# Kernel optimization log

Measured on AMD Instinct MI355X. Metric: run time of the kernel, lower is better.

Reference implementation:

```python
import jax, jax.numpy as jnp
import numpy as np

NM, C_IN, T, V = 256, 64, 128, 21
C_OUT = 64
N_CONVS = 3  # forward only uses convs[0..2]
EPS_BN = 1e-5


def _build_edges(nm, t):
    # replicates get_hi(): 6x6 incidence (transposed), tiled over NM*T graphs
    inc = np.array([[1, 0, 0, 0, 1, 0],
                    [1, 1, 0, 0, 0, 1],
                    [1, 0, 1, 0, 0, 1],
                    [1, 0, 0, 1, 0, 0],
                    [1, 0, 0, 0, 1, 0],
                    [0, 1, 1, 0, 0, 1]], dtype=np.int64).T
    r_idx, c_idx = np.nonzero(inc)  # row-major order, matches torch nonzero
    g = nm * t                      # num_graphs
    nnz = len(r_idx)                # 14
    row = np.tile(r_idx, g) + np.repeat(np.arange(g), nnz) * 6   # targets (edge-node ids)
    col = np.tile(c_idx, g) + np.repeat(np.arange(g), nnz) * 21  # sources (vertex ids)
    return jnp.asarray(col, jnp.int32), jnp.asarray(row, jnp.int32)


def setup_inputs() -> dict:
    key = jax.random.key(0)
    ks = jax.random.split(key, 8)
    x = jax.random.normal(ks[0], (NM, C_IN, T, V), dtype=jnp.float32)
    src, dst = _build_edges(NM, T)
    s_in = 1.0 / np.sqrt(C_IN)
    s_att = 1.0 / np.sqrt(C_OUT)
    Wl = jax.random.normal(ks[1], (N_CONVS, C_OUT, C_IN), jnp.float32) * s_in
    bl = jnp.zeros((N_CONVS, C_OUT), jnp.float32)
    Wr = jax.random.normal(ks[2], (N_CONVS, C_OUT, C_IN), jnp.float32) * s_in
    br = jnp.zeros((N_CONVS, C_OUT), jnp.float32)
    att = jax.random.normal(ks[3], (N_CONVS, C_OUT), jnp.float32) * s_att
    bias = jnp.zeros((N_CONVS, C_OUT), jnp.float32)
    gamma = jnp.full((C_OUT,), 1e-6, jnp.float32)  # bn_init(self.bn, 1e-6)
    beta = jnp.zeros((C_OUT,), jnp.float32)
    return {"x": x, "src": src, "dst": dst, "Wl": Wl, "bl": bl, "Wr": Wr,
            "br": br, "att": att, "bias": bias, "gamma": gamma, "beta": beta}


def _gatv2(feat, src_all, dst_all, valid, Wl, bl, Wr, br, att, bias, n):
    # GATv2Conv, heads=1: e_ij = att . LeakyReLU(Wl x_j + Wr x_i); softmax over dst
    xl = feat @ Wl.T + bl           # [N, Cout]
    xr = feat @ Wr.T + br           # [N, Cout]
    msg = xl[src_all]               # [E, Cout]
    e = jax.nn.leaky_relu(msg + xr[dst_all], 0.2) @ att  # [E]
    e = jnp.where(valid, e, -1e9)   # removed self-loops excluded
    m = jax.ops.segment_max(e, dst_all, num_segments=n)
    a = jnp.exp(e - m[dst_all]) * valid
    denom = jax.ops.segment_sum(a, dst_all, num_segments=n)
    a = a / denom[dst_all]
    return jax.ops.segment_sum(a[:, None] * msg, dst_all, num_segments=n) + bias


def reference(x, src, dst, Wl, bl, Wr, br, att, bias, gamma, beta):
    nm, c, t, v = x.shape
    n = nm * t * v
    feat = jnp.transpose(x, (0, 2, 3, 1)).reshape(n, c)  # '(nm t v) c'
    # PyG GATv2: remove existing self-loops, then add self-loops for all N nodes
    loop = jnp.arange(n, dtype=src.dtype)
    src_all = jnp.concatenate([src, loop])
    dst_all = jnp.concatenate([dst, loop])
    valid = jnp.concatenate([src != dst, jnp.ones((n,), bool)])
    y = None
    for i in range(N_CONVS):
        z = _gatv2(feat, src_all, dst_all, valid,
                   Wl[i], bl[i], Wr[i], br[i], att[i], bias[i], n)
        y = z if y is None else y + z
    y = y.reshape(nm, C_OUT, t, v)  # matches torch .view on node-major buffer
    # BatchNorm2d (eval, running mean 0 / var 1), gamma initialized to 1e-6
    y = y / jnp.sqrt(1.0 + EPS_BN) * gamma[None, :, None, None] + beta[None, :, None, None]
    return jax.nn.relu(y + x)  # residual identity (in_channels == out_channels)
```

## Files before the change

### kernel.cpp

```cpp
#include <hip/hip_runtime.h>
#include <hip/hip_bf16.h>

#define NMSLICE 2688
#define NMELEMS 172032
#define NNODE   688128
#define NDST    196608
#define BNRS    0.9999950000374996f

typedef __attribute__((ext_vector_type(8))) _Float16 half8;
typedef __attribute__((ext_vector_type(2))) _Float16 half2v;
typedef __attribute__((ext_vector_type(4))) unsigned uintx4;
typedef __attribute__((ext_vector_type(4))) float  floatx4;

__device__ __forceinline__ short h2s(float f) {
    union { _Float16 h; short s; } c;
    c.h = (_Float16)f;
    return c.s;
}

__device__ __forceinline__ void loadrow_h(const short* buf, int row, int cb, half2v* o) {
    #pragma unroll
    for (int h = 0; h < 2; ++h) {
        const int k8 = cb * 2 + h;
        uintx4 v = *reinterpret_cast<const uintx4*>(&buf[row * 64 + ((k8 ^ (row & 7)) << 3)]);
        #pragma unroll
        for (int j = 0; j < 4; ++j) o[h * 4 + j] = __builtin_bit_cast(half2v, v[j]);
    }
}

__device__ __forceinline__ float edot2(const half2v* a, const half2v* xr, const half2v* m) {
    half2v s = { (_Float16)0, (_Float16)0 };
    const half2v c02 = { (_Float16)0.2f, (_Float16)0.2f };
    #pragma unroll
    for (int j = 0; j < 8; ++j) {
        half2v z = m[j] + xr[j];
        z = __builtin_elementwise_max(z, c02 * z);
        s += a[j] * z;
    }
    float e = (float)s[0] + (float)s[1];
    e += __shfl_xor(e, 1);
    e += __shfl_xor(e, 2);
    return e;
}

__global__ void __launch_bounds__(256) prep_weights(
    const float* __restrict__ Wl, const float* __restrict__ Wr,
    const float* __restrict__ bl, const float* __restrict__ bias,
    const float* __restrict__ att,
    short* __restrict__ wfrag, float* __restrict__ csum, float* __restrict__ bsum,
    short* __restrict__ att_h)
{
    const int task = blockIdx.x * 256 + threadIdx.x;
    const int lane = task & 63;
    const int ks   = (task >> 6) & 1;
    const int nt   = (task >> 7) & 3;
    const int m    = task >> 9;
    const int co = nt * 16 + (lane & 15);
    const int k0 = ks * 32 + (lane >> 4) * 8;
    short v[8];
    if (m < 6) {
        const int cv = m >> 1;
        const float* W = (m & 1) ? (Wr + cv * 4096) : (Wl + cv * 4096);
        #pragma unroll
        for (int j = 0; j < 8; ++j) v[j] = h2s(W[co * 64 + k0 + j]);
    } else {
        #pragma unroll
        for (int j = 0; j < 8; ++j)
            v[j] = h2s(Wl[co*64 + k0 + j] + Wl[4096 + co*64 + k0 + j] + Wl[8192 + co*64 + k0 + j]);
    }
    #pragma unroll
    for (int j = 0; j < 8; ++j) wfrag[task * 8 + j] = v[j];
    if (blockIdx.x == 0 && threadIdx.x < 192) {
        const int t = threadIdx.x;
        att_h[t] = h2s(att[t]);
        if (t < 64) {
            csum[t] = bl[t] + bl[64+t] + bl[128+t] + bias[t] + bias[64+t] + bias[128+t];
            bsum[t] = bias[t] + bias[64+t] + bias[128+t];
        }
    }
}

__global__ void __launch_bounds__(256) gat_heavy(
    const float* __restrict__ x,
    const short* __restrict__ wfrag,
    const float* __restrict__ bl, const float* __restrict__ br,
    const short* __restrict__ att_h, const float* __restrict__ bsum,
    const float* __restrict__ gamma, const float* __restrict__ beta,
    float* __restrict__ out)
{
    __shared__ short XL[4 * 48 * 64];
    __shared__ short XR[4 * 24 * 64];

    const int lane = threadIdx.x & 63;
    const int wave = threadIdx.x >> 6;
    const int sbid = ((blockIdx.x & 7) << 8) + (blockIdx.x >> 3);
    const int W  = sbid * 4 + wave;
    const int n0 = W * 24;
    const int s0 = W * 84;

    short* XLw = XL + wave * (48 * 64);
    short* XRw = XR + wave * (24 * 64);

    const int nmD = n0 / NMSLICE, rmD = n0 - nmD * NMSLICE;
    const int nmS = s0 / NMSLICE, rmS = s0 - nmS * NMSLICE;

    #pragma unroll
    for (int i = 0; i < 6; ++i) {
        const int task = i * 64 + lane;
        const int r  = task % 48;
        const int k8 = task / 48;
        const float* bp;
        if (r < 24) {
            bp = x + (size_t)nmD * NMELEMS + rmD + r;
        } else {
            const int s = r - 24, gl = s / 6;
            bp = x + (size_t)nmS * NMELEMS + rmS + gl * 21 + (s - gl * 6);
        }
        short v[8];
        #pragma unroll
        for (int j = 0; j < 8; ++j) v[j] = h2s(bp[(size_t)(k8 * 8 + j) * NMSLICE]);
        *reinterpret_cast<half8*>(&XLw[r * 64 + ((k8 ^ (r & 7)) << 3)]) =
            *reinterpret_cast<half8*>(v);
    }

    const int l15 = lane & 15, l4 = lane >> 4;

    half8 aA[3][2];
    #pragma unroll
    for (int t = 0; t < 3; ++t) {
        const int arow = t * 16 + l15;
        #pragma unroll
        for (int ks = 0; ks < 2; ++ks)
            aA[t][ks] = *reinterpret_cast<const half8*>(
                &XLw[arow * 64 + (((ks * 4 + l4) ^ (arow & 7)) << 3)]);
    }

    const int ndA = lane >> 2, cbA = lane & 3;
    const int ndB = 16 + (lane >> 2), cbB = lane & 3;
    const unsigned long long TBL =
        31ull | (34ull << 8) | (36ull << 16) | (8ull << 24) | (17ull << 32) | (38ull << 40);
    const int glA = ndA / 6, rrA = ndA - glA * 6, srowA = 24 + glA * 6;
    const int glB = ndB / 6, rrB = ndB - glB * 6, srowB = 24 + glB * 6;
    unsigned maskA = (unsigned)((TBL >> (rrA * 8)) & 63u);
    unsigned maskB = (unsigned)((TBL >> (rrB * 8)) & 63u);
    if (W == 0 && glA == 0) maskA &= ~(1u << rrA);

    half2v yA2[8], yB2[8];
    #pragma unroll
    for (int j = 0; j < 8; ++j) {
        yA2[j] = half2v{ (_Float16)0, (_Float16)0 };
        yB2[j] = half2v{ (_Float16)0, (_Float16)0 };
    }

    for (int cv = 0; cv < 3; ++cv) {
        #pragma unroll
        for (int nt = 0; nt < 4; ++nt) {
            const int co = nt * 16 + l15;
            const short* wbL = wfrag + (size_t)(((cv * 2    ) * 4 + nt) * 2) * 512;
            const short* wbR = wfrag + (size_t)(((cv * 2 + 1) * 4 + nt) * 2) * 512;
            half8 wl0 = *reinterpret_cast<const half8*>(wbL + lane * 8);
            half8 wl1 = *reinterpret_cast<const half8*>(wbL + 512 + lane * 8);
            half8 wr0 = *reinterpret_cast<const half8*>(wbR + lane * 8);
            half8 wr1 = *reinterpret_cast<const half8*>(wbR + 512 + lane * 8);
            const float biL = bl[cv * 64 + co];
            const float biR = br[cv * 64 + co];
            #pragma unroll
            for (int u = 0; u < 3; ++u) {
                floatx4 acc = { biL, biL, biL, biL };
                acc = __builtin_amdgcn_mfma_f32_16x16x32_f16(aA[u][0], wl0, acc, 0, 0, 0);
                acc = __builtin_amdgcn_mfma_f32_16x16x32_f16(aA[u][1], wl1, acc, 0, 0, 0);
                #pragma unroll
                for (int qq = 0; qq < 4; ++qq) {
                    const int row = u * 16 + l4 * 4 + qq;
                    XLw[row * 64 + (((co >> 3) ^ (row & 7)) << 3) + (co & 7)] = h2s(acc[qq]);
                }
            }
            #pragma unroll
            for (int mtx = 0; mtx < 2; ++mtx) {
                floatx4 acc = { biR, biR, biR, biR };
                acc = __builtin_amdgcn_mfma_f32_16x16x32_f16(aA[mtx][0], wr0, acc, 0, 0, 0);
                acc = __builtin_amdgcn_mfma_f32_16x16x32_f16(aA[mtx][1], wr1, acc, 0, 0, 0);
                #pragma unroll
                for (int qq = 0; qq < 4; ++qq) {
                    const int row = mtx * 16 + l4 * 4 + qq;
                    if (row < 24)
                        XRw[row * 64 + (((co >> 3) ^ (row & 7)) << 3) + (co & 7)] = h2s(acc[qq]);
                }
            }
        }

        {
            half2v a2[8], xr2[8], m2[8], o2[8];
            {
                const uintx4* ap = reinterpret_cast<const uintx4*>(att_h + cv * 64 + cbA * 16);
                uintx4 v0 = ap[0], v1 = ap[1];
                #pragma unroll
                for (int j = 0; j < 4; ++j) {
                    a2[j]     = __builtin_bit_cast(half2v, v0[j]);
                    a2[4 + j] = __builtin_bit_cast(half2v, v1[j]);
                }
            }
            loadrow_h(XRw, ndA, cbA, xr2);
            loadrow_h(XLw, ndA, cbA, m2);
            float e = edot2(a2, xr2, m2);
            float w = __expf(e);
            float denom = w;
            half2v w2 = { (_Float16)w, (_Float16)w };
            #pragma unroll
            for (int j = 0; j < 8; ++j) o2[j] = w2 * m2[j];
            #pragma unroll
            for (int c = 0; c < 6; ++c) {
                loadrow_h(XLw, srowA + c, cbA, m2);
                e = edot2(a2, xr2, m2);
                w = (maskA & (1u << c)) ? __expf(e) : 0.f;
                denom += w;
                w2[0] = (_Float16)w; w2[1] = (_Float16)w;
                #pragma unroll
                for (int j = 0; j < 8; ++j) o2[j] += w2 * m2[j];
            }
            const _Float16 invh = (_Float16)(1.0f / denom);
            const half2v inv2 = { invh, invh };
            #pragma unroll
            for (int j = 0; j < 8; ++j) yA2[j] += inv2 * o2[j];
        }
        if (lane < 32) {
            half2v a2[8], xr2[8], m2[8], o2[8];
            {
                const uintx4* ap = reinterpret_cast<const uintx4*>(att_h + cv * 64 + cbB * 16);
                uintx4 v0 = ap[0], v1 = ap[1];
                #pragma unroll
                for (int j = 0; j < 4; ++j) {
                    a2[j]     = __builtin_bit_cast(half2v, v0[j]);
                    a2[4 + j] = __builtin_bit_cast(half2v, v1[j]);
                }
            }
            loadrow_h(XRw, ndB, cbB, xr2);
            loadrow_h(XLw, ndB, cbB, m2);
            float e = edot2(a2, xr2, m2);
            float w = __expf(e);
            float denom = w;
            half2v w2 = { (_Float16)w, (_Float16)w };
            #pragma unroll
            for (int j = 0; j < 8; ++j) o2[j] = w2 * m2[j];
            #pragma unroll
            for (int c = 0; c < 6; ++c) {
                loadrow_h(XLw, srowB + c, cbB, m2);
                e = edot2(a2, xr2, m2);
                w = (maskB & (1u << c)) ? __expf(e) : 0.f;
                denom += w;
                w2[0] = (_Float16)w; w2[1] = (_Float16)w;
                #pragma unroll
                for (int j = 0; j < 8; ++j) o2[j] += w2 * m2[j];
            }
            const _Float16 invh = (_Float16)(1.0f / denom);
            const half2v inv2 = { invh, invh };
            #pragma unroll
            for (int j = 0; j < 8; ++j) yB2[j] += inv2 * o2[j];
        }
    }

    {
        const size_t i0 = (size_t)(n0 + ndA) * 64 + cbA * 16;
        const int cobn = ((rmD + ndA) * 64 + cbA * 16) / NMSLICE;
        const float sc = gamma[cobn] * BNRS;
        const float bt = beta[cobn];
        #pragma unroll
        for (int j4 = 0; j4 < 4; ++j4) {
            floatx4 xv = *reinterpret_cast<const floatx4*>(x + i0 + j4 * 4);
            floatx4 ov;
            #pragma unroll
            for (int j = 0; j < 4; ++j) {
                const int jj = j4 * 4 + j;
                const float yv = (float)yA2[jj >> 1][jj & 1];
                float val = fmaf(yv + bsum[cbA * 16 + jj], sc, bt) + xv[j];
                ov[j] = fmaxf(val, 0.f);
            }
            *reinterpret_cast<floatx4*>(out + i0 + j4 * 4) = ov;
        }
    }
    if (lane < 32) {
        const size_t i0 = (size_t)(n0 + ndB) * 64 + cbB * 16;
        const int cobn = ((rmD + ndB) * 64 + cbB * 16) / NMSLICE;
        const float sc = gamma[cobn] * BNRS;
        const float bt = beta[cobn];
        #pragma unroll
        for (int j4 = 0; j4 < 4; ++j4) {
            floatx4 xv = *reinterpret_cast<const floatx4*>(x + i0 + j4 * 4);
            floatx4 ov;
            #pragma unroll
            for (int j = 0; j < 4; ++j) {
                const int jj = j4 * 4 + j;
                const float yv = (float)yB2[jj >> 1][jj & 1];
                float val = fmaf(yv + bsum[cbB * 16 + jj], sc, bt) + xv[j];
                ov[j] = fmaxf(val, 0.f);
            }
            *reinterpret_cast<floatx4*>(out + i0 + j4 * 4) = ov;
        }
    }
}

__global__ void __launch_bounds__(256) gat_light(
    const float* __restrict__ x,
    const short* __restrict__ wfrag,
    const float* __restrict__ csum,
    const float* __restrict__ gamma, const float* __restrict__ beta,
    float* __restrict__ out)
{
    __shared__ short F[256 * 64];

    const int t  = threadIdx.x;
    const int n0 = NDST + blockIdx.x * 256;

    {
        const int node = n0 + t;
        const int nm = node / NMSLICE;
        const int rm = node - nm * NMSLICE;
        const float* bp = x + (size_t)nm * NMELEMS + rm;
        #pragma unroll
        for (int k8 = 0; k8 < 8; ++k8) {
            short v[8];
            #pragma unroll
            for (int j = 0; j < 8; ++j) v[j] = h2s(bp[(size_t)(k8 * 8 + j) * NMSLICE]);
            *reinterpret_cast<half8*>(&F[t * 64 + ((k8 ^ (t & 7)) << 3)]) =
                *reinterpret_cast<half8*>(v);
        }
    }
    __syncthreads();

    const int wave = t >> 6, lane = t & 63;
    const int l15 = lane & 15, l4 = lane >> 4;
    const int rm0 = n0 % NMSLICE;
    #pragma unroll
    for (int ti = 0; ti < 16; ++ti) {
        const int tile = wave * 16 + ti;
        const int mt = tile >> 2, nt = tile & 3;
        const int co = nt * 16 + l15;
        const float bi = csum[co];
        floatx4 acc = { bi, bi, bi, bi };
        const short* wbase = wfrag + (size_t)((6 * 4 + nt) * 2) * 512;
        const int arow = mt * 16 + l15;
        #pragma unroll
        for (int ks = 0; ks < 2; ++ks) {
            half8 bfr = *reinterpret_cast<const half8*>(wbase + ks * 512 + lane * 8);
            const int k8 = ks * 4 + l4;
            half8 afr = *reinterpret_cast<const half8*>(
                &F[arow * 64 + ((k8 ^ (arow & 7)) << 3)]);
            acc = __builtin_amdgcn_mfma_f32_16x16x32_f16(afr, bfr, acc, 0, 0, 0);
        }
        #pragma unroll
        for (int qq = 0; qq < 4; ++qq) {
            const int row = mt * 16 + l4 * 4 + qq;
            int rm = rm0 + row; if (rm >= NMSLICE) rm -= NMSLICE;
            const int cobn = (rm * 64 + co) / NMSLICE;
            const size_t fi = (size_t)(n0 + row) * 64 + co;
            const float val = fmaf(acc[qq], gamma[cobn] * BNRS, beta[cobn]) + x[fi];
            out[fi] = fmaxf(val, 0.f);
        }
    }
}

extern "C" void kernel_launch(void* const* d_in, const int* in_sizes, int n_in,
                              void* d_out, int out_size, void* d_ws, size_t ws_size,
                              hipStream_t stream) {
    const float* x     = (const float*)d_in[0];
    const float* Wl    = (const float*)d_in[3];
    const float* bl    = (const float*)d_in[4];
    const float* Wr    = (const float*)d_in[5];
    const float* br    = (const float*)d_in[6];
    const float* att   = (const float*)d_in[7];
    const float* bias  = (const float*)d_in[8];
    const float* gamma = (const float*)d_in[9];
    const float* beta  = (const float*)d_in[10];
    float* out = (float*)d_out;

    short* wfrag = (short*)d_ws;
    float* csum  = (float*)((char*)d_ws + 57344);
    float* bsum  = csum + 64;
    short* att_h = (short*)(bsum + 64);

    hipLaunchKernelGGL(prep_weights, dim3(14), dim3(256), 0, stream,
                       Wl, Wr, bl, bias, att, wfrag, csum, bsum, att_h);
    hipLaunchKernelGGL(gat_heavy, dim3(2048), dim3(256), 0, stream,
                       x, wfrag, bl, br, att_h, bsum, gamma, beta, out);
    hipLaunchKernelGGL(gat_light, dim3(1920), dim3(256), 0, stream,
                       x, wfrag, csum, gamma, beta, out);
}
```

Before: 179.8 us.

## Merge heavy and light GAT kernels into one launch with interleaved block roles

The separate heavy (attention) and light (self-loop-only matmul) kernels become a single kernel. Its grid is split into groups of 31 blocks: 16 take the heavy path and 15 take the light path. This removes one launch and the tail and idle gap between the two kernels, and lets the compute-heavy and memory-bound blocks share the GPU at the same time. In exchange, the shared-memory footprint becomes the max of both paths (heavy needs about 36KB), which may lower occupancy for the light blocks. It also adds a divergent branch at block level.

```diff
diff --git a/kernel.cpp b/kernel.cpp
--- a/kernel.cpp
+++ b/kernel.cpp
@@ -80,281 +80,276 @@
     }
 }
 
-__global__ void __launch_bounds__(256) gat_heavy(
+__global__ void __launch_bounds__(256) gat_fused(
     const float* __restrict__ x,
     const short* __restrict__ wfrag,
     const float* __restrict__ bl, const float* __restrict__ br,
     const short* __restrict__ att_h, const float* __restrict__ bsum,
-    const float* __restrict__ gamma, const float* __restrict__ beta,
-    float* __restrict__ out)
-{
-    __shared__ short XL[4 * 48 * 64];
-    __shared__ short XR[4 * 24 * 64];
-
-    const int lane = threadIdx.x & 63;
-    const int wave = threadIdx.x >> 6;
-    const int sbid = ((blockIdx.x & 7) << 8) + (blockIdx.x >> 3);
-    const int W  = sbid * 4 + wave;
-    const int n0 = W * 24;
-    const int s0 = W * 84;
-
-    short* XLw = XL + wave * (48 * 64);
-    short* XRw = XR + wave * (24 * 64);
-
-    const int nmD = n0 / NMSLICE, rmD = n0 - nmD * NMSLICE;
-    const int nmS = s0 / NMSLICE, rmS = s0 - nmS * NMSLICE;
-
-    #pragma unroll
-    for (int i = 0; i < 6; ++i) {
-        const int task = i * 64 + lane;
-        const int r  = task % 48;
-        const int k8 = task / 48;
-        const float* bp;
-        if (r < 24) {
-            bp = x + (size_t)nmD * NMELEMS + rmD + r;
-        } else {
-            const int s = r - 24, gl = s / 6;
-            bp = x + (size_t)nmS * NMELEMS + rmS + gl * 21 + (s - gl * 6);
-        }
-        short v[8];
-        #pragma unroll
-        for (int j = 0; j < 8; ++j) v[j] = h2s(bp[(size_t)(k8 * 8 + j) * NMSLICE]);
-        *reinterpret_cast<half8*>(&XLw[r * 64 + ((k8 ^ (r & 7)) << 3)]) =
-            *reinterpret_cast<half8*>(v);
-    }
-
-    const int l15 = lane & 15, l4 = lane >> 4;
-
-    half8 aA[3][2];
-    #pragma unroll
-    for (int t = 0; t < 3; ++t) {
-        const int arow = t * 16 + l15;
-        #pragma unroll
-        for (int ks = 0; ks < 2; ++ks)
-            aA[t][ks] = *reinterpret_cast<const half8*>(
-                &XLw[arow * 64 + (((ks * 4 + l4) ^ (arow & 7)) << 3)]);
-    }
-
-    const int ndA = lane >> 2, cbA = lane & 3;
-    const int ndB = 16 + (lane >> 2), cbB = lane & 3;
-    const unsigned long long TBL =
-        31ull | (34ull << 8) | (36ull << 16) | (8ull << 24) | (17ull << 32) | (38ull << 40);
-    const int glA = ndA / 6, rrA = ndA - glA * 6, srowA = 24 + glA * 6;
-    const int glB = ndB / 6, rrB = ndB - glB * 6, srowB = 24 + glB * 6;
-    unsigned maskA = (unsigned)((TBL >> (rrA * 8)) & 63u);
-    unsigned maskB = (unsigned)((TBL >> (rrB * 8)) & 63u);
-    if (W == 0 && glA == 0) maskA &= ~(1u << rrA);
-
-    half2v yA2[8], yB2[8];
-    #pragma unroll
-    for (int j = 0; j < 8; ++j) {
-        yA2[j] = half2v{ (_Float16)0, (_Float16)0 };
-        yB2[j] = half2v{ (_Float16)0, (_Float16)0 };
-    }
-
-    for (int cv = 0; cv < 3; ++cv) {
-        #pragma unroll
-        for (int nt = 0; nt < 4; ++nt) {
-            const int co = nt * 16 + l15;
-            const short* wbL = wfrag + (size_t)(((cv * 2    ) * 4 + nt) * 2) * 512;
-            const short* wbR = wfrag + (size_t)(((cv * 2 + 1) * 4 + nt) * 2) * 512;
-            half8 wl0 = *reinterpret_cast<const half8*>(wbL + lane * 8);
-            half8 wl1 = *reinterpret_cast<const half8*>(wbL + 512 + lane * 8);
-            half8 wr0 = *reinterpret_cast<const half8*>(wbR + lane * 8);
-            half8 wr1 = *reinterpret_cast<const half8*>(wbR + 512 + lane * 8);
-            const float biL = bl[cv * 64 + co];
-            const float biR = br[cv * 64 + co];
-            #pragma unroll
-            for (int u = 0; u < 3; ++u) {
-                floatx4 acc = { biL, biL, biL, biL };
-                acc = __builtin_amdgcn_mfma_f32_16x16x32_f16(aA[u][0], wl0, acc, 0, 0, 0);
-                acc = __builtin_amdgcn_mfma_f32_16x16x32_f16(aA[u][1], wl1, acc, 0, 0, 0);
-                #pragma unroll
-                for (int qq = 0; qq < 4; ++qq) {
-                    const int row = u * 16 + l4 * 4 + qq;
-                    XLw[row * 64 + (((co >> 3) ^ (row & 7)) << 3) + (co & 7)] = h2s(acc[qq]);
-                }
-            }
-            #pragma unroll
-            for (int mtx = 0; mtx < 2; ++mtx) {
-                floatx4 acc = { biR, biR, biR, biR };
-                acc = __builtin_amdgcn_mfma_f32_16x16x32_f16(aA[mtx][0], wr0, acc, 0, 0, 0);
-                acc = __builtin_amdgcn_mfma_f32_16x16x32_f16(aA[mtx][1], wr1, acc, 0, 0, 0);
-                #pragma unroll
-                for (int qq = 0; qq < 4; ++qq) {
-                    const int row = mtx * 16 + l4 * 4 + qq;
-                    if (row < 24)
-                        XRw[row * 64 + (((co >> 3) ^ (row & 7)) << 3) + (co & 7)] = h2s(acc[qq]);
-                }
-            }
-        }
-
-        {
-            half2v a2[8], xr2[8], m2[8], o2[8];
-            {
-                const uintx4* ap = reinterpret_cast<const uintx4*>(att_h + cv * 64 + cbA * 16);
-                uintx4 v0 = ap[0], v1 = ap[1];
-                #pragma unroll
-                for (int j = 0; j < 4; ++j) {
-                    a2[j]     = __builtin_bit_cast(half2v, v0[j]);
-                    a2[4 + j] = __builtin_bit_cast(half2v, v1[j]);
-                }
-            }
-            loadrow_h(XRw, ndA, cbA, xr2);
-            loadrow_h(XLw, ndA, cbA, m2);
-            float e = edot2(a2, xr2, m2);
-            float w = __expf(e);
-            float denom = w;
-            half2v w2 = { (_Float16)w, (_Float16)w };
-            #pragma unroll
-            for (int j = 0; j < 8; ++j) o2[j] = w2 * m2[j];
-            #pragma unroll
-            for (int c = 0; c < 6; ++c) {
-                loadrow_h(XLw, srowA + c, cbA, m2);
-                e = edot2(a2, xr2, m2);
-                w = (maskA & (1u << c)) ? __expf(e) : 0.f;
-                denom += w;
-                w2[0] = (_Float16)w; w2[1] = (_Float16)w;
-                #pragma unroll
-                for (int j = 0; j < 8; ++j) o2[j] += w2 * m2[j];
-            }
-            const _Float16 invh = (_Float16)(1.0f / denom);
-            const half2v inv2 = { invh, invh };
-            #pragma unroll
-            for (int j = 0; j < 8; ++j) yA2[j] += inv2 * o2[j];
-        }
-        if (lane < 32) {
-            half2v a2[8], xr2[8], m2[8], o2[8];
-            {
-                const uintx4* ap = reinterpret_cast<const uintx4*>(att_h + cv * 64 + cbB * 16);
-                uintx4 v0 = ap[0], v1 = ap[1];
-                #pragma unroll
-                for (int j = 0; j < 4; ++j) {
-                    a2[j]     = __builtin_bit_cast(half2v, v0[j]);
-                    a2[4 + j] = __builtin_bit_cast(half2v, v1[j]);
-                }
-            }
-            loadrow_h(XRw, ndB, cbB, xr2);
-            loadrow_h(XLw, ndB, cbB, m2);
-            float e = edot2(a2, xr2, m2);
-            float w = __expf(e);
-            float denom = w;
-            half2v w2 = { (_Float16)w, (_Float16)w };
-            #pragma unroll
-            for (int j = 0; j < 8; ++j) o2[j] = w2 * m2[j];
-            #pragma unroll
-            for (int c = 0; c < 6; ++c) {
-                loadrow_h(XLw, srowB + c, cbB, m2);
-                e = edot2(a2, xr2, m2);
-                w = (maskB & (1u << c)) ? __expf(e) : 0.f;
-                denom += w;
-                w2[0] = (_Float16)w; w2[1] = (_Float16)w;
-                #pragma unroll
-                for (int j = 0; j < 8; ++j) o2[j] += w2 * m2[j];
-            }
-            const _Float16 invh = (_Float16)(1.0f / denom);
-            const half2v inv2 = { invh, invh };
-            #pragma unroll
-            for (int j = 0; j < 8; ++j) yB2[j] += inv2 * o2[j];
-        }
-    }
-
-    {
-        const size_t i0 = (size_t)(n0 + ndA) * 64 + cbA * 16;
-        const int cobn = ((rmD + ndA) * 64 + cbA * 16) / NMSLICE;
-        const float sc = gamma[cobn] * BNRS;
-        const float bt = beta[cobn];
-        #pragma unroll
-        for (int j4 = 0; j4 < 4; ++j4) {
-            floatx4 xv = *reinterpret_cast<const floatx4*>(x + i0 + j4 * 4);
-            floatx4 ov;
-            #pragma unroll
-            for (int j = 0; j < 4; ++j) {
-                const int jj = j4 * 4 + j;
-                const float yv = (float)yA2[jj >> 1][jj & 1];
-                float val = fmaf(yv + bsum[cbA * 16 + jj], sc, bt) + xv[j];
-                ov[j] = fmaxf(val, 0.f);
-            }
-            *reinterpret_cast<floatx4*>(out + i0 + j4 * 4) = ov;
-        }
-    }
-    if (lane < 32) {
-        const size_t i0 = (size_t)(n0 + ndB) * 64 + cbB * 16;
-        const int cobn = ((rmD + ndB) * 64 + cbB * 16) / NMSLICE;
-        const float sc = gamma[cobn] * BNRS;
-        const float bt = beta[cobn];
-        #pragma unroll
-        for (int j4 = 0; j4 < 4; ++j4) {
-            floatx4 xv = *reinterpret_cast<const floatx4*>(x + i0 + j4 * 4);
-            floatx4 ov;
-            #pragma unroll
-            for (int j = 0; j < 4; ++j) {
-                const int jj = j4 * 4 + j;
-                const float yv = (float)yB2[jj >> 1][jj & 1];
-                float val = fmaf(yv + bsum[cbB * 16 + jj], sc, bt) + xv[j];
-                ov[j] = fmaxf(val, 0.f);
-            }
-            *reinterpret_cast<floatx4*>(out + i0 + j4 * 4) = ov;
-        }
-    }
-}
-
-__global__ void __launch_bounds__(256) gat_light(
-    const float* __restrict__ x,
-    const short* __restrict__ wfrag,
     const float* __restrict__ csum,
     const float* __restrict__ gamma, const float* __restrict__ beta,
     float* __restrict__ out)
 {
-    __shared__ short F[256 * 64];
-
-    const int t  = threadIdx.x;
-    const int n0 = NDST + blockIdx.x * 256;
-
-    {
-        const int node = n0 + t;
-        const int nm = node / NMSLICE;
-        const int rm = node - nm * NMSLICE;
-        const float* bp = x + (size_t)nm * NMELEMS + rm;
-        #pragma unroll
-        for (int k8 = 0; k8 < 8; ++k8) {
+    __shared__ short SM[4 * 48 * 64 + 4 * 24 * 64];
+
+    const int lane = threadIdx.x & 63;
+    const int wave = threadIdx.x >> 6;
+    const int l15 = lane & 15, l4 = lane >> 4;
+    const int g31 = blockIdx.x / 31;
+    const int i31 = blockIdx.x - g31 * 31;
+
+    if (i31 < 16) {
+        const int hid = g31 * 16 + i31;
+        const int sbid = ((hid & 7) << 8) + (hid >> 3);
+        const int W  = sbid * 4 + wave;
+        const int n0 = W * 24;
+        const int s0 = W * 84;
+
+        short* XLw = SM + wave * (48 * 64);
+        short* XRw = SM + 4 * 48 * 64 + wave * (24 * 64);
+
+        const int nmD = n0 / NMSLICE, rmD = n0 - nmD * NMSLICE;
+        const int nmS = s0 / NMSLICE, rmS = s0 - nmS * NMSLICE;
+
+        #pragma unroll
+        for (int i = 0; i < 6; ++i) {
+            const int task = i * 64 + lane;
+            const int r  = task % 48;
+            const int k8 = task / 48;
+            const float* bp;
+            if (r < 24) {
+                bp = x + (size_t)nmD * NMELEMS + rmD + r;
+            } else {
+                const int s = r - 24, gl = s / 6;
+                bp = x + (size_t)nmS * NMELEMS + rmS + gl * 21 + (s - gl * 6);
+            }
             short v[8];
             #pragma unroll
             for (int j = 0; j < 8; ++j) v[j] = h2s(bp[(size_t)(k8 * 8 + j) * NMSLICE]);
-            *reinterpret_cast<half8*>(&F[t * 64 + ((k8 ^ (t & 7)) << 3)]) =
+            *reinterpret_cast<half8*>(&XLw[r * 64 + ((k8 ^ (r & 7)) << 3)]) =
                 *reinterpret_cast<half8*>(v);
         }
-    }
-    __syncthreads();
-
-    const int wave = t >> 6, lane = t & 63;
-    const int l15 = lane & 15, l4 = lane >> 4;
-    const int rm0 = n0 % NMSLICE;
-    #pragma unroll
-    for (int ti = 0; ti < 16; ++ti) {
-        const int tile = wave * 16 + ti;
-        const int mt = tile >> 2, nt = tile & 3;
-        const int co = nt * 16 + l15;
-        const float bi = csum[co];
-        floatx4 acc = { bi, bi, bi, bi };
-        const short* wbase = wfrag + (size_t)((6 * 4 + nt) * 2) * 512;
-        const int arow = mt * 16 + l15;
-        #pragma unroll
-        for (int ks = 0; ks < 2; ++ks) {
-            half8 bfr = *reinterpret_cast<const half8*>(wbase + ks * 512 + lane * 8);
-            const int k8 = ks * 4 + l4;
-            half8 afr = *reinterpret_cast<const half8*>(
-                &F[arow * 64 + ((k8 ^ (arow & 7)) << 3)]);
-            acc = __builtin_amdgcn_mfma_f32_16x16x32_f16(afr, bfr, acc, 0, 0, 0);
-        }
-        #pragma unroll
-        for (int qq = 0; qq < 4; ++qq) {
-            const int row = mt * 16 + l4 * 4 + qq;
-            int rm = rm0 + row; if (rm >= NMSLICE) rm -= NMSLICE;
-            const int cobn = (rm * 64 + co) / NMSLICE;
-            const size_t fi = (size_t)(n0 + row) * 64 + co;
-            const float val = fmaf(acc[qq], gamma[cobn] * BNRS, beta[cobn]) + x[fi];
-            out[fi] = fmaxf(val, 0.f);
+
+        half8 aA[3][2];
+        #pragma unroll
+        for (int t = 0; t < 3; ++t) {
+            const int arow = t * 16 + l15;
+            #pragma unroll
+            for (int ks = 0; ks < 2; ++ks)
+                aA[t][ks] = *reinterpret_cast<const half8*>(
+                    &XLw[arow * 64 + (((ks * 4 + l4) ^ (arow & 7)) << 3)]);
+        }
+
+        const int ndA = lane >> 2, cbA = lane & 3;
+        const int ndB = 16 + (lane >> 2), cbB = lane & 3;
+        const unsigned long long TBL =
+            31ull | (34ull << 8) | (36ull << 16) | (8ull << 24) | (17ull << 32) | (38ull << 40);
+        const int glA = ndA / 6, rrA = ndA - glA * 6, srowA = 24 + glA * 6;
+        const int glB = ndB / 6, rrB = ndB - glB * 6, srowB = 24 + glB * 6;
+        unsigned maskA = (unsigned)((TBL >> (rrA * 8)) & 63u);
+        unsigned maskB = (unsigned)((TBL >> (rrB * 8)) & 63u);
+        if (W == 0 && glA == 0) maskA &= ~(1u << rrA);
+
+        half2v yA2[8], yB2[8];
+        #pragma unroll
+        for (int j = 0; j < 8; ++j) {
+            yA2[j] = half2v{ (_Float16)0, (_Float16)0 };
+            yB2[j] = half2v{ (_Float16)0, (_Float16)0 };
+        }
+
+        for (int cv = 0; cv < 3; ++cv) {
+            #pragma unroll
+            for (int nt = 0; nt < 4; ++nt) {
+                const int co = nt * 16 + l15;
+                const short* wbL = wfrag + (size_t)(((cv * 2    ) * 4 + nt) * 2) * 512;
+                const short* wbR = wfrag + (size_t)(((cv * 2 + 1) * 4 + nt) * 2) * 512;
+                half8 wl0 = *reinterpret_cast<const half8*>(wbL + lane * 8);
+                half8 wl1 = *reinterpret_cast<const half8*>(wbL + 512 + lane * 8);
+                half8 wr0 = *reinterpret_cast<const half8*>(wbR + lane * 8);
+                half8 wr1 = *reinterpret_cast<const half8*>(wbR + 512 + lane * 8);
+                const float biL = bl[cv * 64 + co];
+                const float biR = br[cv * 64 + co];
+                #pragma unroll
+                for (int u = 0; u < 3; ++u) {
+                    floatx4 acc = { biL, biL, biL, biL };
+                    acc = __builtin_amdgcn_mfma_f32_16x16x32_f16(aA[u][0], wl0, acc, 0, 0, 0);
+                    acc = __builtin_amdgcn_mfma_f32_16x16x32_f16(aA[u][1], wl1, acc, 0, 0, 0);
+                    #pragma unroll
+                    for (int qq = 0; qq < 4; ++qq) {
+                        const int row = u * 16 + l4 * 4 + qq;
+                        XLw[row * 64 + (((co >> 3) ^ (row & 7)) << 3) + (co & 7)] = h2s(acc[qq]);
+                    }
+                }
+                #pragma unroll
+                for (int mtx = 0; mtx < 2; ++mtx) {
+                    floatx4 acc = { biR, biR, biR, biR };
+                    acc = __builtin_amdgcn_mfma_f32_16x16x32_f16(aA[mtx][0], wr0, acc, 0, 0, 0);
+                    acc = __builtin_amdgcn_mfma_f32_16x16x32_f16(aA[mtx][1], wr1, acc, 0, 0, 0);
+                    #pragma unroll
+                    for (int qq = 0; qq < 4; ++qq) {
+                        const int row = mtx * 16 + l4 * 4 + qq;
+                        if (row < 24)
+                            XRw[row * 64 + (((co >> 3) ^ (row & 7)) << 3) + (co & 7)] = h2s(acc[qq]);
+                    }
+                }
+            }
+
+            {
+                half2v a2[8], xr2[8], m2[8], o2[8];
+                {
+                    const uintx4* ap = reinterpret_cast<const uintx4*>(att_h + cv * 64 + cbA * 16);
+                    uintx4 v0 = ap[0], v1 = ap[1];
+                    #pragma unroll
+                    for (int j = 0; j < 4; ++j) {
+                        a2[j]     = __builtin_bit_cast(half2v, v0[j]);
+                        a2[4 + j] = __builtin_bit_cast(half2v, v1[j]);
+                    }
+                }
+                loadrow_h(XRw, ndA, cbA, xr2);
+                loadrow_h(XLw, ndA, cbA, m2);
+                float e = edot2(a2, xr2, m2);
+                float w = __expf(e);
+                float denom = w;
+                half2v w2 = { (_Float16)w, (_Float16)w };
+                #pragma unroll
+                for (int j = 0; j < 8; ++j) o2[j] = w2 * m2[j];
+                #pragma unroll
+                for (int c = 0; c < 6; ++c) {
+                    loadrow_h(XLw, srowA + c, cbA, m2);
+                    e = edot2(a2, xr2, m2);
+                    w = (maskA & (1u << c)) ? __expf(e) : 0.f;
+                    denom += w;
+                    w2[0] = (_Float16)w; w2[1] = (_Float16)w;
+                    #pragma unroll
+                    for (int j = 0; j < 8; ++j) o2[j] += w2 * m2[j];
+                }
+                const _Float16 invh = (_Float16)(1.0f / denom);
+                const half2v inv2 = { invh, invh };
+                #pragma unroll
+                for (int j = 0; j < 8; ++j) yA2[j] += inv2 * o2[j];
+            }
+            if (lane < 32) {
+                half2v a2[8], xr2[8], m2[8], o2[8];
+                {
+                    const uintx4* ap = reinterpret_cast<const uintx4*>(att_h + cv * 64 + cbB * 16);
+                    uintx4 v0 = ap[0], v1 = ap[1];
+                    #pragma unroll
+                    for (int j = 0; j < 4; ++j) {
+                        a2[j]     = __builtin_bit_cast(half2v, v0[j]);
+                        a2[4 + j] = __builtin_bit_cast(half2v, v1[j]);
+                    }
+                }
+                loadrow_h(XRw, ndB, cbB, xr2);
+                loadrow_h(XLw, ndB, cbB, m2);
+                float e = edot2(a2, xr2, m2);
+                float w = __expf(e);
+                float denom = w;
+                half2v w2 = { (_Float16)w, (_Float16)w };
+                #pragma unroll
+                for (int j = 0; j < 8; ++j) o2[j] = w2 * m2[j];
+                #pragma unroll
+                for (int c = 0; c < 6; ++c) {
+                    loadrow_h(XLw, srowB + c, cbB, m2);
+                    e = edot2(a2, xr2, m2);
+                    w = (maskB & (1u << c)) ? __expf(e) : 0.f;
+                    denom += w;
+                    w2[0] = (_Float16)w; w2[1] = (_Float16)w;
+                    #pragma unroll
+                    for (int j = 0; j < 8; ++j) o2[j] += w2 * m2[j];
+                }
+                const _Float16 invh = (_Float16)(1.0f / denom);
+                const half2v inv2 = { invh, invh };
+                #pragma unroll
+                for (int j = 0; j < 8; ++j) yB2[j] += inv2 * o2[j];
+            }
+        }
+
+        {
+            const size_t i0 = (size_t)(n0 + ndA) * 64 + cbA * 16;
+            const int cobn = ((rmD + ndA) * 64 + cbA * 16) / NMSLICE;
+            const float sc = gamma[cobn] * BNRS;
+            const float bt = beta[cobn];
+            #pragma unroll
+            for (int j4 = 0; j4 < 4; ++j4) {
+                floatx4 xv = *reinterpret_cast<const floatx4*>(x + i0 + j4 * 4);
+                floatx4 ov;
+                #pragma unroll
+                for (int j = 0; j < 4; ++j) {
+                    const int jj = j4 * 4 + j;
+                    const float yv = (float)yA2[jj >> 1][jj & 1];
+                    float val = fmaf(yv + bsum[cbA * 16 + jj], sc, bt) + xv[j];
+                    ov[j] = fmaxf(val, 0.f);
+                }
+                *reinterpret_cast<floatx4*>(out + i0 + j4 * 4) = ov;
+            }
+        }
+        if (lane < 32) {
+            const size_t i0 = (size_t)(n0 + ndB) * 64 + cbB * 16;
+            const int cobn = ((rmD + ndB) * 64 + cbB * 16) / NMSLICE;
+            const float sc = gamma[cobn] * BNRS;
+            const float bt = beta[cobn];
+            #pragma unroll
+            for (int j4 = 0; j4 < 4; ++j4) {
+                floatx4 xv = *reinterpret_cast<const floatx4*>(x + i0 + j4 * 4);
+                floatx4 ov;
+                #pragma unroll
+                for (int j = 0; j < 4; ++j) {
+                    const int jj = j4 * 4 + j;
+                    const float yv = (float)yB2[jj >> 1][jj & 1];
+                    float val = fmaf(yv + bsum[cbB * 16 + jj], sc, bt) + xv[j];
+                    ov[j] = fmaxf(val, 0.f);
+                }
+                *reinterpret_cast<floatx4*>(out + i0 + j4 * 4) = ov;
+            }
+        }
+    } else {
+        const int lid = g31 * 15 + (i31 - 16);
+        const int t  = threadIdx.x;
+        const int n0 = NDST + lid * 256;
+        short* F = SM;
+
+        {
+            const int node = n0 + t;
+            const int nm = node / NMSLICE;
+            const int rm = node - nm * NMSLICE;
+            const float* bp = x + (size_t)nm * NMELEMS + rm;
+            #pragma unroll
+            for (int k8 = 0; k8 < 8; ++k8) {
+                short v[8];
+                #pragma unroll
+                for (int j = 0; j < 8; ++j) v[j] = h2s(bp[(size_t)(k8 * 8 + j) * NMSLICE]);
+                *reinterpret_cast<half8*>(&F[t * 64 + ((k8 ^ (t & 7)) << 3)]) =
+                    *reinterpret_cast<half8*>(v);
+            }
+        }
+        __syncthreads();
+
+        const int rm0 = n0 % NMSLICE;
+        #pragma unroll
+        for (int ti = 0; ti < 16; ++ti) {
+            const int tile = wave * 16 + ti;
+            const int mt = tile >> 2, nt = tile & 3;
+            const int co = nt * 16 + l15;
+            const float bi = csum[co];
+            floatx4 acc = { bi, bi, bi, bi };
+            const short* wbase = wfrag + (size_t)((6 * 4 + nt) * 2) * 512;
+            const int arow = mt * 16 + l15;
+            #pragma unroll
+            for (int ks = 0; ks < 2; ++ks) {
+                half8 bfr = *reinterpret_cast<const half8*>(wbase + ks * 512 + lane * 8);
+                const int k8 = ks * 4 + l4;
+                half8 afr = *reinterpret_cast<const half8*>(
+                    &F[arow * 64 + ((k8 ^ (arow & 7)) << 3)]);
+                acc = __builtin_amdgcn_mfma_f32_16x16x32_f16(afr, bfr, acc, 0, 0, 0);
+            }
+            #pragma unroll
+            for (int qq = 0; qq < 4; ++qq) {
+                const int row = mt * 16 + l4 * 4 + qq;
+                int rm = rm0 + row; if (rm >= NMSLICE) rm -= NMSLICE;
+                const int cobn = (rm * 64 + co) / NMSLICE;
+                const size_t fi = (size_t)(n0 + row) * 64 + co;
+                const float val = fmaf(acc[qq], gamma[cobn] * BNRS, beta[cobn]) + x[fi];
+                out[fi] = fmaxf(val, 0.f);
+            }
         }
     }
 }
@@ -380,8 +375,6 @@
 
     hipLaunchKernelGGL(prep_weights, dim3(14), dim3(256), 0, stream,
                        Wl, Wr, bl, bias, att, wfrag, csum, bsum, att_h);
-    hipLaunchKernelGGL(gat_heavy, dim3(2048), dim3(256), 0, stream,
-                       x, wfrag, bl, br, att_h, bsum, gamma, beta, out);
-    hipLaunchKernelGGL(gat_light, dim3(1920), dim3(256), 0, stream,
-                       x, wfrag, csum, gamma, beta, out);
-}
+    hipLaunchKernelGGL(gat_fused, dim3(128 * 31), dim3(256), 0, stream,
+                       x, wfrag, bl, br, att_h, bsum, csum, gamma, beta, out);
+}
```

New measurement: 292.6 us. 1.63x slower.
